# Kernel tuning notes

Measured on AMD Instinct MI355X. Metric: run time of the kernel, lower is better.

## Reference

```python
import jax, jax.numpy as jnp
import numpy as np

B, S, E, H = 4, 2048, 1024, 16
D = E // H  # head_dim = 64

def setup_inputs() -> dict:
    key = jax.random.key(0)
    k1, k2, k3, k4, k5 = jax.random.split(key, 5)
    x = jax.random.normal(k1, (B, S, E), dtype=jnp.float32)
    # causal mask, broadcast over batch and heads; mask==0 -> -inf
    mask = jnp.tril(jnp.ones((S, S), dtype=jnp.int32))[None, None, :, :]
    Wqkv = jax.random.normal(k2, (E, 3 * E), dtype=jnp.float32) * (1.0 / np.sqrt(E))
    bqkv = jax.random.normal(k3, (3 * E,), dtype=jnp.float32) * 0.02
    Wo = jax.random.normal(k4, (E, E), dtype=jnp.float32) * (1.0 / np.sqrt(E))
    bo = jax.random.normal(k5, (E,), dtype=jnp.float32) * 0.02
    return {"x": x, "mask": mask, "Wqkv": Wqkv, "bqkv": bqkv, "Wo": Wo, "bo": bo}

def reference(x, mask, Wqkv, bqkv, Wo, bo):
    b, s, e = x.shape
    scale = 1.0 / np.sqrt(D)
    qkv = x @ Wqkv + bqkv                      # [b,s,3e]
    qkv = qkv.reshape(b, s, H, 3 * D).transpose(0, 2, 1, 3)  # [b,h,s,3d]
    q, k, v = jnp.split(qkv, 3, axis=-1)       # each [b,h,s,d]
    scores = jnp.einsum('bnqd,bnkd->bnqk', q, k) * scale
    scores = jnp.where(mask == 0, -jnp.inf, scores)
    probs = jax.nn.softmax(scores, axis=-1)
    attn = jnp.einsum('bnqk,bnkd->bnqd', probs, v)  # [b,h,s,d]
    # Faithful to source: reshape (b,h,s,d) -> (b,s,e) WITHOUT transposing back
    attn = attn.reshape(b, s, e)
    return attn @ Wo + bo
```

## Files before the change

kernel.cpp:

```cpp
#include <hip/hip_runtime.h>

typedef __attribute__((ext_vector_type(8))) short bf16x8;
typedef __attribute__((ext_vector_type(4))) float f32x4;
typedef __attribute__((ext_vector_type(2))) unsigned int u32x2;
typedef __attribute__((ext_vector_type(4))) unsigned int u32x4;

#define MFMA16(a, b, c) __builtin_amdgcn_mfma_f32_16x16x32_bf16((a), (b), (c), 0, 0, 0)

#define S_LEN 2048
#define NHEAD 16
#define DHEAD 64
#define BH    64
#define MROWS 8192

__device__ __forceinline__ unsigned short f2bf(float f) {
  unsigned int u = __builtin_bit_cast(unsigned int, f);
  u += 0x7FFFu + ((u >> 16) & 1u);
  return (unsigned short)(u >> 16);
}

__device__ __forceinline__ void gl_lds16(const void* g, void* l) {
  __builtin_amdgcn_global_load_lds(
      (const __attribute__((address_space(1))) void*)g,
      (__attribute__((address_space(3))) void*)l, 16, 0, 0);
}

__device__ __forceinline__ unsigned int pkbf(float lo, float hi) {
  unsigned int ulo = __builtin_bit_cast(unsigned int, lo) + 0x8000u;
  unsigned int uhi = __builtin_bit_cast(unsigned int, hi) + 0x8000u;
  return __builtin_amdgcn_perm(uhi, ulo, 0x07060302u);
}

__global__ __launch_bounds__(256) void prep(const float* __restrict__ x,
                                            unsigned short* __restrict__ Xbf,
                                            const float* __restrict__ Wqkv,
                                            unsigned short* __restrict__ WqkvT,
                                            const float* __restrict__ Wo,
                                            unsigned short* __restrict__ WoT) {
  __shared__ float tile[32][33];
  const int bid = blockIdx.x;
  const int tid = threadIdx.x;
  if (bid < 8192) {
    int i = (bid * 256 + tid) * 4;
    f32x4 v = *(const f32x4*)(x + i);
    unsigned long long pk =
        (unsigned long long)f2bf(v[0]) |
        ((unsigned long long)f2bf(v[1]) << 16) |
        ((unsigned long long)f2bf(v[2]) << 32) |
        ((unsigned long long)f2bf(v[3]) << 48);
    *(unsigned long long*)(Xbf + i) = pk;
  } else if (bid < 11264) {
    const int b2 = bid - 8192;
    const int c0 = (b2 % 96) * 32, r0 = (b2 / 96) * 32;
    const int tx = tid & 31, ty = tid >> 5;
    for (int i = 0; i < 32; i += 8)
      tile[ty + i][tx] = Wqkv[(size_t)(r0 + ty + i) * 3072 + c0 + tx];
    __syncthreads();
    for (int i = 0; i < 32; i += 8) {
      int oc = c0 + ty + i;
      int h = oc / 192, rr = oc % 192;
      int nc = ((rr >> 6) << 10) + (h << 6) + (rr & 63);
      WqkvT[(size_t)nc * 1024 + r0 + tx] = f2bf(tile[tx][ty + i]);
    }
  } else {
    const int b2 = bid - 11264;
    const int c0 = (b2 & 31) * 32, r0 = (b2 >> 5) * 32;
    const int tx = tid & 31, ty = tid >> 5;
    for (int i = 0; i < 32; i += 8)
      tile[ty + i][tx] = Wo[(size_t)(r0 + ty + i) * 1024 + c0 + tx];
    __syncthreads();
    for (int i = 0; i < 32; i += 8)
      WoT[(size_t)(c0 + ty + i) * 1024 + r0 + tx] = f2bf(tile[tx][ty + i]);
  }
}


#define VM3 asm volatile("s_waitcnt vmcnt(3)" ::: "memory")
#define VM0 asm volatile("s_waitcnt vmcnt(0)" ::: "memory")
#define BAR __builtin_amdgcn_s_barrier()
#define SB  __builtin_amdgcn_sched_barrier(0)
#define SGB_G(m, n) __builtin_amdgcn_sched_group_barrier((m), (n), 0)

#define SGBPAT                                                                   \
  SGB_G(0x70, 3);                                                                \
  SGB_G(0x8, 2); SGB_G(0x100, 1); SGB_G(0x8, 2); SGB_G(0x100, 1);                \
  SGB_G(0x8, 2); SGB_G(0x100, 1); SGB_G(0x8, 2); SGB_G(0x100, 1);                \
  SGB_G(0x8, 2); SGB_G(0x100, 1); SGB_G(0x8, 2); SGB_G(0x100, 1);                \
  SGB_G(0x8, 2); SGB_G(0x100, 1); SGB_G(0x8, 2); SGB_G(0x100, 1)

#define STAGE3(T, KH, BUF)                                                       \
  do {                                                                           \
    const unsigned short* ga_ = a_src + (T) * 64 + (KH) * 32;                    \
    const unsigned short* gb_ = b_src + (T) * 64 + (KH) * 32;                    \
    char* la_ = SHB + (BUF) * 49152 + (KH) * 8192 + stgo;                        \
    char* lb_ = SHB + (BUF) * 49152 + 16384 + (KH) * 16384 + stgo;               \
    gl_lds16(ga_, la_);                                                          \
    gl_lds16(gb_, lb_);                                                          \
    gl_lds16(gb_ + 131072, lb_ + 8192);                                          \
  } while (0)

#define RDSET(S, BUF, KH)                                                        \
  do {                                                                           \
    const char* Ab_ = SHB + (BUF) * 49152 + (KH) * 8192 + abase;                 \
    const char* Bb_ = SHB + (BUF) * 49152 + 16384 + (KH) * 16384 + bbase;        \
    af##S##0 = *(const bf16x8*)(Ab_);                                            \
    af##S##1 = *(const bf16x8*)(Ab_ + 1024);                                     \
    af##S##2 = *(const bf16x8*)(Ab_ + 2048);                                     \
    af##S##3 = *(const bf16x8*)(Ab_ + 3072);                                     \
    bq##S##0 = *(const bf16x8*)(Bb_);                                            \
    bq##S##1 = *(const bf16x8*)(Bb_ + 1024);                                     \
    bq##S##2 = *(const bf16x8*)(Bb_ + 2048);                                     \
    bq##S##3 = *(const bf16x8*)(Bb_ + 3072);                                     \
  } while (0)

#define MFMA16S(S)                                                               \
  acc[0][0] = MFMA16(af##S##0, bq##S##0, acc[0][0]);                             \
  acc[0][1] = MFMA16(af##S##0, bq##S##1, acc[0][1]);                             \
  acc[0][2] = MFMA16(af##S##0, bq##S##2, acc[0][2]);                             \
  acc[0][3] = MFMA16(af##S##0, bq##S##3, acc[0][3]);                             \
  acc[1][0] = MFMA16(af##S##1, bq##S##0, acc[1][0]);                             \
  acc[1][1] = MFMA16(af##S##1, bq##S##1, acc[1][1]);                             \
  acc[1][2] = MFMA16(af##S##1, bq##S##2, acc[1][2]);                             \
  acc[1][3] = MFMA16(af##S##1, bq##S##3, acc[1][3]);                             \
  acc[2][0] = MFMA16(af##S##2, bq##S##0, acc[2][0]);                             \
  acc[2][1] = MFMA16(af##S##2, bq##S##1, acc[2][1]);                             \
  acc[2][2] = MFMA16(af##S##2, bq##S##2, acc[2][2]);                             \
  acc[2][3] = MFMA16(af##S##2, bq##S##3, acc[2][3]);                             \
  acc[3][0] = MFMA16(af##S##3, bq##S##0, acc[3][0]);                             \
  acc[3][1] = MFMA16(af##S##3, bq##S##1, acc[3][1]);                             \
  acc[3][2] = MFMA16(af##S##3, bq##S##2, acc[3][2]);                             \
  acc[3][3] = MFMA16(af##S##3, bq##S##3, acc[3][3])

#define WND(SP, STG_, VM_, RD_)                                                  \
  {                                                                              \
    STG_;                                                                        \
    __builtin_amdgcn_s_setprio(1);                                               \
    MFMA16S(SP);                                                                 \
    RD_;                                                                         \
    __builtin_amdgcn_s_setprio(0);                                               \
    SGBPAT;                                                                      \
    VM_; SB; BAR; SB;                                                            \
  }

#define GEMM256_KLOOP                                                            \
  STAGE3(0, 0, 0); STAGE3(0, 1, 0); STAGE3(1, 0, 1);                             \
  VM3; SB; BAR; SB;                                                              \
  RDSET(A, 0, 0);                                                                \
  _Pragma("unroll 1")                                                            \
  for (int jj = 0; jj < 7; ++jj) {                                               \
    const int J0 = 2 * jj;                                                       \
    WND(A, STAGE3(J0 + 1, 1, 1), VM3, RDSET(B, 0, 1))                            \
    WND(B, STAGE3(J0 + 2, 0, 0), VM3, RDSET(A, 1, 0))                            \
    WND(A, STAGE3(J0 + 2, 1, 0), VM3, RDSET(B, 1, 1))                            \
    WND(B, STAGE3(J0 + 3, 0, 1), VM3, RDSET(A, 0, 0))                            \
  }                                                                              \
  WND(A, STAGE3(15, 1, 1), VM3, RDSET(B, 0, 1))                                  \
  WND(B, (void)0, VM0, RDSET(A, 1, 0))                                           \
  WND(A, (void)0, (void)0, RDSET(B, 1, 1))                                       \
  __builtin_amdgcn_s_setprio(1);                                                 \
  MFMA16S(B);                                                                    \
  __builtin_amdgcn_s_setprio(0);                                                 \
  __syncthreads();

__global__ __launch_bounds__(512, 2) void gemm_qkv(const unsigned short* __restrict__ A,
                                                   const unsigned short* __restrict__ Bt,
                                                   const float* __restrict__ bias,
                                                   unsigned short* __restrict__ Qb,
                                                   unsigned short* __restrict__ Kb,
                                                   unsigned short* __restrict__ Vtb) {
  __shared__ unsigned short SH[49152];
  char* SHB = (char*)SH;
  const int tid = threadIdx.x;
  const int w = tid >> 6, lane = tid & 63, l15 = lane & 15, quad = lane >> 4;
  const int wm = w >> 2, wn = w & 3;
  const int g = ((blockIdx.x & 7) * 96) + (blockIdx.x >> 3);
  const int bx = g % 12, by = g / 12;
  const int col0 = bx << 8, row0 = by << 7;

  const int qa = quad ^ ((l15 >> 1) & 3);
  const int abase = (wm * 64 + l15) * 64 + qa * 16;
  const int bbase = (wn * 64 + l15) * 64 + qa * 16;

  const int qsw = (tid & 3) ^ ((tid >> 3) & 3);
  const unsigned short* a_src = A + (size_t)(row0 + (tid >> 2)) * 1024 + qsw * 8;
  const unsigned short* b_src = Bt + (size_t)(col0 + (tid >> 2)) * 1024 + qsw * 8;
  const int stgo = (tid & ~63) * 16;

  f32x4 acc[4][4] = {};
  bf16x8 afA0, afA1, afA2, afA3, bqA0, bqA1, bqA2, bqA3;
  bf16x8 afB0, afB1, afB2, afB3, bqB0, bqB1, bqB2, bqB3;

  GEMM256_KLOOP

  const int which = col0 >> 10;
  const int h = ((col0 + wn * 64) >> 6) & 15;
  const int b = row0 >> 11;
  const int srow0 = (row0 & 2047) + wm * 64;
  float bv[4];
  #pragma unroll
  for (int j = 0; j < 4; ++j) {
    int nc = col0 + wn * 64 + j * 16 + l15;
    int oc = ((nc >> 6) & 15) * 192 + (nc >> 10) * 64 + (nc & 63);
    bv[j] = bias[oc];
  }
  float* Ew = (float*)SHB + w * 1072;

  if (which < 2) {
    const float sc = (which == 0) ? 0.18033688011112042f : 1.0f;
    const int lr = lane >> 2, d0 = (lane & 3) * 16;
    unsigned short* base = (which == 0 ? Qb : Kb) + ((size_t)(b * 16 + h) * 2048 + srow0) * 64;
    #pragma unroll
    for (int i = 0; i < 4; ++i) {
      #pragma unroll
      for (int j = 0; j < 4; ++j)
        #pragma unroll
        for (int r = 0; r < 4; ++r)
          Ew[(quad * 4 + r) * 66 + j * 16 + l15] = (acc[i][j][r] + bv[j]) * sc;
      float v[16];
      #pragma unroll
      for (int c = 0; c < 4; ++c)
        *(f32x4*)&v[4 * c] = *(const f32x4*)&Ew[lr * 66 + d0 + 4 * c];
      u32x4 pk0 = {pkbf(v[0], v[1]), pkbf(v[2], v[3]), pkbf(v[4], v[5]), pkbf(v[6], v[7])};
      u32x4 pk1 = {pkbf(v[8], v[9]), pkbf(v[10], v[11]), pkbf(v[12], v[13]), pkbf(v[14], v[15])};
      unsigned short* dst = base + (size_t)(i * 16 + lr) * 64 + d0;
      *(u32x4*)dst = pk0;
      *(u32x4*)(dst + 8) = pk1;
    }
  } else {
    const int d = lane;
    unsigned short* base = Vtb + ((size_t)(b * 16 + h) * 64 + d) * 2048 + srow0;
    #pragma unroll
    for (int i = 0; i < 4; ++i) {
      #pragma unroll
      for (int j = 0; j < 4; ++j)
        #pragma unroll
        for (int r = 0; r < 4; ++r)
          Ew[(quad * 4 + r) * 66 + j * 16 + l15] = acc[i][j][r] + bv[j];
      float e[16];
      #pragma unroll
      for (int k = 0; k < 16; ++k) e[k] = Ew[k * 66 + d];
      u32x4 pk0 = {pkbf(e[0], e[1]), pkbf(e[2], e[3]), pkbf(e[4], e[5]), pkbf(e[6], e[7])};
      u32x4 pk1 = {pkbf(e[8], e[9]), pkbf(e[10], e[11]), pkbf(e[12], e[13]), pkbf(e[14], e[15])};
      unsigned short* dst = base + i * 16;
      *(u32x4*)dst = pk0;
      *(u32x4*)(dst + 8) = pk1;
    }
  }
}

__global__ __launch_bounds__(512, 2) void gemm_out(const unsigned short* __restrict__ A,
                                                   const unsigned short* __restrict__ Bt,
                                                   const float* __restrict__ bias,
                                                   float* __restrict__ out) {
  __shared__ unsigned short SH[49152];
  char* SHB = (char*)SH;
  const int tid = threadIdx.x;
  const int w = tid >> 6, lane = tid & 63, l15 = lane & 15, quad = lane >> 4;
  const int wm = w >> 2, wn = w & 3;
  const int g = ((blockIdx.x & 7) * 32) + (blockIdx.x >> 3);
  const int bx = g & 3, by = g >> 2;
  const int col0 = bx << 8, row0 = by << 7;

  const int qa = quad ^ ((l15 >> 1) & 3);
  const int abase = (wm * 64 + l15) * 64 + qa * 16;
  const int bbase = (wn * 64 + l15) * 64 + qa * 16;

  const int qsw = (tid & 3) ^ ((tid >> 3) & 3);
  const unsigned short* a_src = A + (size_t)(row0 + (tid >> 2)) * 1024 + qsw * 8;
  const unsigned short* b_src = Bt + (size_t)(col0 + (tid >> 2)) * 1024 + qsw * 8;
  const int stgo = (tid & ~63) * 16;

  f32x4 acc[4][4] = {};
  bf16x8 afA0, afA1, afA2, afA3, bqA0, bqA1, bqA2, bqA3;
  bf16x8 afB0, afB1, afB2, afB3, bqB0, bqB1, bqB2, bqB3;

  GEMM256_KLOOP

  const int grow0 = row0 + wm * 64;
  const int gcol0 = col0 + wn * 64;
  #pragma unroll
  for (int i = 0; i < 4; ++i) {
    #pragma unroll
    for (int j = 0; j < 4; ++j) {
      const int gcol = gcol0 + j * 16 + l15;
      const float bvv = bias[gcol];
      #pragma unroll
      for (int r = 0; r < 4; ++r)
        out[(size_t)(grow0 + i * 16 + quad * 4 + r) * 1024 + gcol] = acc[i][j][r] + bvv;
    }
  }
}

__global__ __launch_bounds__(256, 3) void attn_kernel(const unsigned short* __restrict__ Qb,
                                                      const unsigned short* __restrict__ Kb,
                                                      const unsigned short* __restrict__ Vtb,
                                                      unsigned short* __restrict__ attnout) {
  __shared__ unsigned short K0[2][64 * 32], K1[2][64 * 32];
  __shared__ unsigned short V0[2][64 * 32], V1[2][64 * 32];
  __shared__ unsigned short P0[4][2][512], P1[4][2][512];
  __shared__ float Lbc[4][32];

  const int tid = threadIdx.x;
  const int w = tid >> 6, lane = tid & 63, l15 = lane & 15, quad = lane >> 4;
  const int i2 = blockIdx.x >> 6;
  const int a = i2 & 3, kq = i2 >> 2;
  const int qt = (kq == 0) ? a : (kq == 1) ? (15 - a) : (kq == 2) ? (7 - a) : (8 + a);
  const int bh = blockIdx.x & 63;
  const int q0w = qt * 128 + w * 32;

  const unsigned short* Qg = Qb + (size_t)bh * S_LEN * DHEAD;
  const unsigned short* Kg = Kb + (size_t)bh * S_LEN * DHEAD;
  const unsigned short* Vg = Vtb + (size_t)bh * DHEAD * S_LEN;

  bf16x8 qf[2][2];
  #pragma unroll
  for (int sub = 0; sub < 2; ++sub) {
    const unsigned short* p = Qg + (size_t)(q0w + sub * 16 + l15) * DHEAD + quad * 8;
    qf[sub][0] = *(const bf16x8*)p;
    qf[sub][1] = *(const bf16x8*)(p + 32);
  }

  const int srow = tid >> 2, sc8 = (tid & 3) * 8;
  const unsigned short* kgb = Kg + srow * 64 + sc8;
  const unsigned short* vgb = Vg + (size_t)srow * S_LEN + sc8;
  const int wKo = srow * 32 + sc8;

  const int psw = (l15 & 3) ^ ((l15 >> 2) & 3);
  const int pw0 = l15 * 32 + (((quad >> 1) ^ psw) << 3) + ((quad & 1) << 2);
  const int pw1 = l15 * 32 + ((((quad >> 1) + 2) ^ psw) << 3) + ((quad & 1) << 2);
  const int pro = l15 * 32 + ((quad ^ psw) << 3);
  const int kvo = l15 * 32 + quad * 8;

  f32x4 oacc[2][4] = {};
  float lacc[2] = {0.f, 0.f};

  const int ktdiag = 2 * qt;
  const int nkt = ktdiag + 2;

  bf16x8 kr0 = *(const bf16x8*)kgb, kr1 = *(const bf16x8*)(kgb + 32);
  bf16x8 vr0 = *(const bf16x8*)vgb, vr1 = *(const bf16x8*)(vgb + 32);
  *(bf16x8*)&K0[0][wKo] = kr0;  *(bf16x8*)&K1[0][wKo] = kr1;
  *(bf16x8*)&V0[0][wKo] = vr0;  *(bf16x8*)&V1[0][wKo] = vr1;
  {
    const unsigned short* kp = kgb + 4096;
    const unsigned short* vp = vgb + 64;
    kr0 = *(const bf16x8*)kp;  kr1 = *(const bf16x8*)(kp + 32);
    vr0 = *(const bf16x8*)vp;  vr1 = *(const bf16x8*)(vp + 32);
  }
  __syncthreads();

  for (int kt = 0; kt < nkt; ++kt) {
    const int cur = kt & 1, nxt = cur ^ 1;
    if (kt + 1 < nkt) {
      *(bf16x8*)&K0[nxt][wKo] = kr0;  *(bf16x8*)&K1[nxt][wKo] = kr1;
      *(bf16x8*)&V0[nxt][wKo] = vr0;  *(bf16x8*)&V1[nxt][wKo] = vr1;
      if (kt + 2 < nkt) {
        const unsigned short* kp = kgb + (kt + 2) * 4096;
        const unsigned short* vp = vgb + (kt + 2) * 64;
        kr0 = *(const bf16x8*)kp;  kr1 = *(const bf16x8*)(kp + 32);
        vr0 = *(const bf16x8*)vp;  vr1 = *(const bf16x8*)(vp + 32);
      }
    }
    const unsigned short* Kc0 = K0[cur];
    const unsigned short* Kc1 = K1[cur];
    const unsigned short* Vc0 = V0[cur];
    const unsigned short* Vc1 = V1[cur];

    const int t = kt - ktdiag;
    const int dgw = w - 2 * t;
    const bool act = (t < 0) || (dgw >= 0);

    if (act) {
      if (t < 0 || dgw >= 2) {
        #pragma unroll
        for (int jk = 0; jk < 4; ++jk) {
          bf16x8 kf0 = *(const bf16x8*)&Kc0[jk * 512 + kvo];
          bf16x8 kf1 = *(const bf16x8*)&Kc1[jk * 512 + kvo];
          #pragma unroll
          for (int sub = 0; sub < 2; ++sub) {
            f32x4 z = {};
            z = MFMA16(kf0, qf[sub][0], z);
            z = MFMA16(kf1, qf[sub][1], z);
            float e0 = __builtin_amdgcn_exp2f(z[0]);
            float e1 = __builtin_amdgcn_exp2f(z[1]);
            float e2 = __builtin_amdgcn_exp2f(z[2]);
            float e3 = __builtin_amdgcn_exp2f(z[3]);
            lacc[sub] += (e0 + e1) + (e2 + e3);
            unsigned short* pd = (jk < 2) ? P0[w][sub] : P1[w][sub];
            *(u32x2*)&pd[(jk & 1) ? pw1 : pw0] = (u32x2){pkbf(e0, e1), pkbf(e2, e3)};
          }
        }
      } else {
        #pragma unroll
        for (int jk = 0; jk < 4; ++jk) {
          bf16x8 kf0 = *(const bf16x8*)&Kc0[jk * 512 + kvo];
          bf16x8 kf1 = *(const bf16x8*)&Kc1[jk * 512 + kvo];
          #pragma unroll
          for (int sub = 0; sub < 2; ++sub) {
            const int m = dgw * 2 + sub;
            unsigned short* pd = (jk < 2) ? P0[w][sub] : P1[w][sub];
            unsigned int* dst = (unsigned int*)&pd[(jk & 1) ? pw1 : pw0];
            if (jk > m) { *(u32x2*)dst = (u32x2){0u, 0u}; continue; }
            f32x4 z = {};
            z = MFMA16(kf0, qf[sub][0], z);
            z = MFMA16(kf1, qf[sub][1], z);
            if (jk == m) {
              #pragma unroll
              for (int r = 0; r < 4; ++r)
                if (quad * 4 + r > l15) z[r] = -3e38f;
            }
            float e0 = __builtin_amdgcn_exp2f(z[0]);
            float e1 = __builtin_amdgcn_exp2f(z[1]);
            float e2 = __builtin_amdgcn_exp2f(z[2]);
            float e3 = __builtin_amdgcn_exp2f(z[3]);
            lacc[sub] += (e0 + e1) + (e2 + e3);
            *(u32x2*)dst = (u32x2){pkbf(e0, e1), pkbf(e2, e3)};
          }
        }
      }

      bf16x8 pf[2][2];
      #pragma unroll
      for (int sub = 0; sub < 2; ++sub) {
        pf[sub][0] = *(const bf16x8*)&P0[w][sub][pro];
        pf[sub][1] = *(const bf16x8*)&P1[w][sub][pro];
      }
      #pragma unroll
      for (int dt = 0; dt < 4; ++dt) {
        bf16x8 vb0 = *(const bf16x8*)&Vc0[dt * 512 + kvo];
        bf16x8 vb1 = *(const bf16x8*)&Vc1[dt * 512 + kvo];
        #pragma unroll
        for (int sub = 0; sub < 2; ++sub) {
          oacc[sub][dt] = MFMA16(pf[sub][0], vb0, oacc[sub][dt]);
          oacc[sub][dt] = MFMA16(pf[sub][1], vb1, oacc[sub][dt]);
        }
      }
    }
    __syncthreads();
  }

  #pragma unroll
  for (int sub = 0; sub < 2; ++sub) {
    float l = lacc[sub];
    l += __shfl_xor(l, 16);
    l += __shfl_xor(l, 32);
    if (quad == 0) Lbc[w][sub * 16 + l15] = l;
  }
  __builtin_amdgcn_s_barrier();
  #pragma unroll
  for (int sub = 0; sub < 2; ++sub) {
    f32x4 l4 = *(const f32x4*)&Lbc[w][sub * 16 + quad * 4];
    int qbase = q0w + sub * 16 + quad * 4;
    unsigned short* dst = attnout + ((size_t)bh * S_LEN + qbase) * DHEAD;
    #pragma unroll
    for (int r = 0; r < 4; ++r) {
      float inv = __builtin_amdgcn_rcpf(l4[r]);
      #pragma unroll
      for (int dt = 0; dt < 4; ++dt)
        dst[(size_t)r * DHEAD + dt * 16 + l15] = f2bf(oacc[sub][dt][r] * inv);
    }
  }
}

extern "C" void kernel_launch(void* const* d_in, const int* in_sizes, int n_in,
                              void* d_out, int out_size, void* d_ws, size_t ws_size,
                              hipStream_t stream) {
  const float* x    = (const float*)d_in[0];
  const float* Wqkv = (const float*)d_in[2];
  const float* bqkv = (const float*)d_in[3];
  const float* Wo   = (const float*)d_in[4];
  const float* bo   = (const float*)d_in[5];
  float* out = (float*)d_out;

  char* ws = (char*)d_ws;
  unsigned short* Xbf   = (unsigned short*)(ws);
  unsigned short* WqkvT = (unsigned short*)(ws + 16777216);
  unsigned short* WoT   = (unsigned short*)(ws + 23068672);
  unsigned short* Qb    = (unsigned short*)(ws + 25165824);
  unsigned short* Kb    = (unsigned short*)(ws + 41943040);
  unsigned short* Vtb   = (unsigned short*)(ws + 58720256);
  unsigned short* Attn  = (unsigned short*)(ws + 75497472);

  prep<<<12288, 256, 0, stream>>>(x, Xbf, Wqkv, WqkvT, Wo, WoT);
  gemm_qkv<<<768, 512, 0, stream>>>(Xbf, WqkvT, bqkv, Qb, Kb, Vtb);
  attn_kernel<<<1024, 256, 0, stream>>>(Qb, Kb, Vtb, Attn);
  gemm_out<<<256, 512, 0, stream>>>(Attn, WoT, bo, out);
}
```

Measured before the change: 257.4 us.

## Widen QKV GEMM tile to 128x384 with 12 waves per block

```diff
diff --git a/kernel.cpp b/kernel.cpp
--- a/kernel.cpp
+++ b/kernel.cpp
@@ -74,8 +74,8 @@
   }
 }
 
-
 #define VM3 asm volatile("s_waitcnt vmcnt(3)" ::: "memory")
+#define VM2 asm volatile("s_waitcnt vmcnt(2)" ::: "memory")
 #define VM0 asm volatile("s_waitcnt vmcnt(0)" ::: "memory")
 #define BAR __builtin_amdgcn_s_barrier()
 #define SB  __builtin_amdgcn_sched_barrier(0)
@@ -87,31 +87,6 @@
   SGB_G(0x8, 2); SGB_G(0x100, 1); SGB_G(0x8, 2); SGB_G(0x100, 1);                \
   SGB_G(0x8, 2); SGB_G(0x100, 1); SGB_G(0x8, 2); SGB_G(0x100, 1);                \
   SGB_G(0x8, 2); SGB_G(0x100, 1); SGB_G(0x8, 2); SGB_G(0x100, 1)
-
-#define STAGE3(T, KH, BUF)                                                       \
-  do {                                                                           \
-    const unsigned short* ga_ = a_src + (T) * 64 + (KH) * 32;                    \
-    const unsigned short* gb_ = b_src + (T) * 64 + (KH) * 32;                    \
-    char* la_ = SHB + (BUF) * 49152 + (KH) * 8192 + stgo;                        \
-    char* lb_ = SHB + (BUF) * 49152 + 16384 + (KH) * 16384 + stgo;               \
-    gl_lds16(ga_, la_);                                                          \
-    gl_lds16(gb_, lb_);                                                          \
-    gl_lds16(gb_ + 131072, lb_ + 8192);                                          \
-  } while (0)
-
-#define RDSET(S, BUF, KH)                                                        \
-  do {                                                                           \
-    const char* Ab_ = SHB + (BUF) * 49152 + (KH) * 8192 + abase;                 \
-    const char* Bb_ = SHB + (BUF) * 49152 + 16384 + (KH) * 16384 + bbase;        \
-    af##S##0 = *(const bf16x8*)(Ab_);                                            \
-    af##S##1 = *(const bf16x8*)(Ab_ + 1024);                                     \
-    af##S##2 = *(const bf16x8*)(Ab_ + 2048);                                     \
-    af##S##3 = *(const bf16x8*)(Ab_ + 3072);                                     \
-    bq##S##0 = *(const bf16x8*)(Bb_);                                            \
-    bq##S##1 = *(const bf16x8*)(Bb_ + 1024);                                     \
-    bq##S##2 = *(const bf16x8*)(Bb_ + 2048);                                     \
-    bq##S##3 = *(const bf16x8*)(Bb_ + 3072);                                     \
-  } while (0)
 
 #define MFMA16S(S)                                                               \
   acc[0][0] = MFMA16(af##S##0, bq##S##0, acc[0][0]);                             \
@@ -141,6 +116,31 @@
     SGBPAT;                                                                      \
     VM_; SB; BAR; SB;                                                            \
   }
+
+#define STAGE3(T, KH, BUF)                                                       \
+  do {                                                                           \
+    const unsigned short* ga_ = a_src + (T) * 64 + (KH) * 32;                    \
+    const unsigned short* gb_ = b_src + (T) * 64 + (KH) * 32;                    \
+    char* la_ = SHB + (BUF) * 49152 + (KH) * 8192 + stgo;                        \
+    char* lb_ = SHB + (BUF) * 49152 + 16384 + (KH) * 16384 + stgo;               \
+    gl_lds16(ga_, la_);                                                          \
+    gl_lds16(gb_, lb_);                                                          \
+    gl_lds16(gb_ + 131072, lb_ + 8192);                                          \
+  } while (0)
+
+#define RDSET(S, BUF, KH)                                                        \
+  do {                                                                           \
+    const char* Ab_ = SHB + (BUF) * 49152 + (KH) * 8192 + abase;                 \
+    const char* Bb_ = SHB + (BUF) * 49152 + 16384 + (KH) * 16384 + bbase;        \
+    af##S##0 = *(const bf16x8*)(Ab_);                                            \
+    af##S##1 = *(const bf16x8*)(Ab_ + 1024);                                     \
+    af##S##2 = *(const bf16x8*)(Ab_ + 2048);                                     \
+    af##S##3 = *(const bf16x8*)(Ab_ + 3072);                                     \
+    bq##S##0 = *(const bf16x8*)(Bb_);                                            \
+    bq##S##1 = *(const bf16x8*)(Bb_ + 1024);                                     \
+    bq##S##2 = *(const bf16x8*)(Bb_ + 2048);                                     \
+    bq##S##3 = *(const bf16x8*)(Bb_ + 3072);                                     \
+  } while (0)
 
 #define GEMM256_KLOOP                                                            \
   STAGE3(0, 0, 0); STAGE3(0, 1, 0); STAGE3(1, 0, 1);                             \
@@ -162,20 +162,66 @@
   __builtin_amdgcn_s_setprio(0);                                                 \
   __syncthreads();
 
-__global__ __launch_bounds__(512, 2) void gemm_qkv(const unsigned short* __restrict__ A,
+#define STAGE3W(T, KH, BUF)                                                      \
+  do {                                                                           \
+    if (tid < 512) {                                                             \
+      const unsigned short* ga_ = a_src + (T) * 64 + (KH) * 32;                  \
+      gl_lds16(ga_, SHB + (BUF) * 65536 + (KH) * 8192 + stgoA);                  \
+    }                                                                            \
+    const unsigned short* gb_ = b_src + (T) * 64 + (KH) * 32;                    \
+    char* lb_ = SHB + (BUF) * 65536 + 16384 + (KH) * 24576 + stgoB;              \
+    gl_lds16(gb_, lb_);                                                          \
+    gl_lds16(gb_ + 196608, lb_ + 12288);                                         \
+  } while (0)
+
+#define RDSETW(S, BUF, KH)                                                       \
+  do {                                                                           \
+    const char* Ab_ = SHB + (BUF) * 65536 + (KH) * 8192 + abase;                 \
+    const char* Bb_ = SHB + (BUF) * 65536 + 16384 + (KH) * 24576 + bbase;        \
+    af##S##0 = *(const bf16x8*)(Ab_);                                            \
+    af##S##1 = *(const bf16x8*)(Ab_ + 1024);                                     \
+    af##S##2 = *(const bf16x8*)(Ab_ + 2048);                                     \
+    af##S##3 = *(const bf16x8*)(Ab_ + 3072);                                     \
+    bq##S##0 = *(const bf16x8*)(Bb_);                                            \
+    bq##S##1 = *(const bf16x8*)(Bb_ + 1024);                                     \
+    bq##S##2 = *(const bf16x8*)(Bb_ + 2048);                                     \
+    bq##S##3 = *(const bf16x8*)(Bb_ + 3072);                                     \
+  } while (0)
+
+#define GEMM384_KLOOP                                                            \
+  STAGE3W(0, 0, 0); STAGE3W(0, 1, 0); STAGE3W(1, 0, 1);                          \
+  VM2; SB; BAR; SB;                                                              \
+  RDSETW(A, 0, 0);                                                               \
+  _Pragma("unroll 1")                                                            \
+  for (int jj = 0; jj < 7; ++jj) {                                               \
+    const int J0 = 2 * jj;                                                       \
+    WND(A, STAGE3W(J0 + 1, 1, 1), VM2, RDSETW(B, 0, 1))                          \
+    WND(B, STAGE3W(J0 + 2, 0, 0), VM2, RDSETW(A, 1, 0))                          \
+    WND(A, STAGE3W(J0 + 2, 1, 0), VM2, RDSETW(B, 1, 1))                          \
+    WND(B, STAGE3W(J0 + 3, 0, 1), VM2, RDSETW(A, 0, 0))                          \
+  }                                                                              \
+  WND(A, STAGE3W(15, 1, 1), VM2, RDSETW(B, 0, 1))                                \
+  WND(B, (void)0, VM0, RDSETW(A, 1, 0))                                          \
+  WND(A, (void)0, (void)0, RDSETW(B, 1, 1))                                      \
+  __builtin_amdgcn_s_setprio(1);                                                 \
+  MFMA16S(B);                                                                    \
+  __builtin_amdgcn_s_setprio(0);                                                 \
+  __syncthreads();
+
+__global__ __launch_bounds__(768, 3) void gemm_qkv(const unsigned short* __restrict__ A,
                                                    const unsigned short* __restrict__ Bt,
                                                    const float* __restrict__ bias,
                                                    unsigned short* __restrict__ Qb,
                                                    unsigned short* __restrict__ Kb,
                                                    unsigned short* __restrict__ Vtb) {
-  __shared__ unsigned short SH[49152];
+  __shared__ unsigned short SH[65536];
   char* SHB = (char*)SH;
   const int tid = threadIdx.x;
   const int w = tid >> 6, lane = tid & 63, l15 = lane & 15, quad = lane >> 4;
-  const int wm = w >> 2, wn = w & 3;
-  const int g = ((blockIdx.x & 7) * 96) + (blockIdx.x >> 3);
-  const int bx = g % 12, by = g / 12;
-  const int col0 = bx << 8, row0 = by << 7;
+  const int wm = w / 6, wn = w % 6;
+  const int g = ((blockIdx.x & 7) * 64) + (blockIdx.x >> 3);
+  const int bx = g & 7, by = g >> 3;
+  const int col0 = bx * 384, row0 = by << 7;
 
   const int qa = quad ^ ((l15 >> 1) & 3);
   const int abase = (wm * 64 + l15) * 64 + qa * 16;
@@ -184,22 +230,24 @@
   const int qsw = (tid & 3) ^ ((tid >> 3) & 3);
   const unsigned short* a_src = A + (size_t)(row0 + (tid >> 2)) * 1024 + qsw * 8;
   const unsigned short* b_src = Bt + (size_t)(col0 + (tid >> 2)) * 1024 + qsw * 8;
-  const int stgo = (tid & ~63) * 16;
+  const int stgoA = (tid & ~63) * 16;
+  const int stgoB = (tid & ~63) * 16;
 
   f32x4 acc[4][4] = {};
   bf16x8 afA0, afA1, afA2, afA3, bqA0, bqA1, bqA2, bqA3;
   bf16x8 afB0, afB1, afB2, afB3, bqB0, bqB1, bqB2, bqB3;
 
-  GEMM256_KLOOP
-
-  const int which = col0 >> 10;
-  const int h = ((col0 + wn * 64) >> 6) & 15;
+  GEMM384_KLOOP
+
+  const int colw = col0 + wn * 64;
+  const int which = colw >> 10;
+  const int h = (colw >> 6) & 15;
   const int b = row0 >> 11;
   const int srow0 = (row0 & 2047) + wm * 64;
   float bv[4];
   #pragma unroll
   for (int j = 0; j < 4; ++j) {
-    int nc = col0 + wn * 64 + j * 16 + l15;
+    int nc = colw + j * 16 + l15;
     int oc = ((nc >> 6) & 15) * 192 + (nc >> 10) * 64 + (nc & 63);
     bv[j] = bias[oc];
   }
@@ -482,7 +530,7 @@
   unsigned short* Attn  = (unsigned short*)(ws + 75497472);
 
   prep<<<12288, 256, 0, stream>>>(x, Xbf, Wqkv, WqkvT, Wo, WoT);
-  gemm_qkv<<<768, 512, 0, stream>>>(Xbf, WqkvT, bqkv, Qb, Kb, Vtb);
+  gemm_qkv<<<512, 768, 0, stream>>>(Xbf, WqkvT, bqkv, Qb, Kb, Vtb);
   attn_kernel<<<1024, 256, 0, stream>>>(Qb, Kb, Vtb, Attn);
   gemm_out<<<256, 512, 0, stream>>>(Attn, WoT, bo, out);
 }
```

Result: no change. 258.6 us (+0.5%).
